# Kernel tuning notes

Measured on AMD Instinct MI355X. Metric: run time of the kernel, lower is better.

## Reference

```python
import jax, jax.numpy as jnp
import numpy as np


def setup_inputs() -> dict:
    key = jax.random.key(0)
    kq, kk, kv, km = jax.random.split(key, 4)
    B, H, S, D = 2, 16, 2048, 64
    q = jax.random.normal(kq, (B, H, S, D), dtype=jnp.float32)
    k = jax.random.normal(kk, (B, H, S, D), dtype=jnp.float32)
    v = jax.random.normal(kv, (B, H, S, D), dtype=jnp.float32)
    mask = jax.random.randint(km, (B, 1, S, S), 0, 2, dtype=jnp.int32)
    return {"q": q, "k": k, "v": v, "mask": mask}


def reference(q, k, v, mask):
    # Scaled dot-product attention: softmax(Q K^T / sqrt(D)) V
    D = q.shape[-1]
    scale = jnp.asarray(1.0 / np.sqrt(D), q.dtype)
    score = jnp.einsum("bhqd,bhkd->bhqk", q, k) * scale  # [B,H,S,S]
    score = jnp.where(mask == 0, jnp.asarray(-10000.0, score.dtype), score)
    attn = jax.nn.softmax(score, axis=-1)
    out = jnp.einsum("bhqk,bhkd->bhqd", attn, v)  # [B,H,S,D]
    return (out, attn)
```

## Files before the change

kernel.cpp:

```cpp
#include <hip/hip_runtime.h>
#include <stdint.h>

typedef __attribute__((ext_vector_type(8))) short short8;
typedef __attribute__((ext_vector_type(4))) float f32x4;

#define B_ 2
#define H_ 16
#define S_ 2048
#define D_ 64

__device__ __forceinline__ short f2b(float f) {
  unsigned u = __builtin_bit_cast(unsigned, f);
  u += 0x7fffu + ((u >> 16) & 1u);
  return (short)(u >> 16);
}

__global__ __launch_bounds__(256, 4)
void attn_kernel(const float* __restrict__ Q, const float* __restrict__ K,
                 const float* __restrict__ V, const int* __restrict__ M,
                 float* __restrict__ O, float* __restrict__ A)
{
  const int qt   = blockIdx.x;
  const int bh   = blockIdx.y;
  const int b    = bh >> 4;
  const int tid  = threadIdx.x;
  const int wave = tid >> 6;
  const int lane = tid & 63;
  const int l15  = lane & 15;
  const int quad = lane >> 4;

  const float* Qp = Q + (size_t)bh * S_ * D_;
  const float* Kp = K + (size_t)bh * S_ * D_;
  const float* Vp = V + (size_t)bh * S_ * D_;
  const int*   Mp = M + (size_t)b * S_ * S_;
  float* Op = O + (size_t)bh * S_ * D_;
  float* Ap = A + (size_t)bh * S_ * S_;

  const int q0 = qt * 64 + wave * 16;

  __shared__ __attribute__((aligned(16))) short Ks[32][72];
  __shared__ __attribute__((aligned(16))) short Vt[64][40];
  __shared__ __attribute__((aligned(16))) short Ps[4][16][40];

  short8 aq[2];
  {
    const float* qr = Qp + (size_t)(q0 + l15) * D_ + quad * 8;
#pragma unroll
    for (int h = 0; h < 2; ++h) {
      const float4 x0 = *(const float4*)(qr + h * 32);
      const float4 x1 = *(const float4*)(qr + h * 32 + 4);
      aq[h][0] = f2b(x0.x * 0.125f); aq[h][1] = f2b(x0.y * 0.125f);
      aq[h][2] = f2b(x0.z * 0.125f); aq[h][3] = f2b(x0.w * 0.125f);
      aq[h][4] = f2b(x1.x * 0.125f); aq[h][5] = f2b(x1.y * 0.125f);
      aq[h][6] = f2b(x1.z * 0.125f); aq[h][7] = f2b(x1.w * 0.125f);
    }
  }

  const int srow = tid >> 3;
  const int sdc  = (tid & 7) * 8;

  float lsum[4] = {0.f, 0.f, 0.f, 0.f};
  for (int kt = 0; kt < S_; kt += 32) {
    __syncthreads();
    {
      const float* kr = Kp + (size_t)(kt + srow) * D_ + sdc;
      const float4 x0 = *(const float4*)(kr);
      const float4 x1 = *(const float4*)(kr + 4);
      short8 t;
      t[0]=f2b(x0.x); t[1]=f2b(x0.y); t[2]=f2b(x0.z); t[3]=f2b(x0.w);
      t[4]=f2b(x1.x); t[5]=f2b(x1.y); t[6]=f2b(x1.z); t[7]=f2b(x1.w);
      *(short8*)&Ks[srow][sdc] = t;
    }
    __syncthreads();

    f32x4 acc[2] = {{0.f,0.f,0.f,0.f},{0.f,0.f,0.f,0.f}};
#pragma unroll
    for (int nt = 0; nt < 2; ++nt)
#pragma unroll
      for (int h = 0; h < 2; ++h) {
        const short8 bk = *(const short8*)&Ks[nt*16 + l15][h*32 + quad*8];
        acc[nt] = __builtin_amdgcn_mfma_f32_16x16x32_bf16(aq[h], bk, acc[nt], 0, 0, 0);
      }
#pragma unroll
    for (int nt = 0; nt < 2; ++nt)
#pragma unroll
      for (int r = 0; r < 4; ++r) {
        const int row = q0 + quad*4 + r;
        const int col = kt + nt*16 + l15;
        const int m = Mp[(size_t)row * S_ + col];
        lsum[r] += m ? __expf(acc[nt][r]) : 0.f;
      }
  }
#pragma unroll
  for (int r = 0; r < 4; ++r) {
    float s = lsum[r];
    s += __shfl_xor(s, 1);
    s += __shfl_xor(s, 2);
    s += __shfl_xor(s, 4);
    s += __shfl_xor(s, 8);
    lsum[r] = (s > 0.f) ? (1.f / s) : 0.f;
  }

  f32x4 oacc[4] = {{0.f,0.f,0.f,0.f},{0.f,0.f,0.f,0.f},
                   {0.f,0.f,0.f,0.f},{0.f,0.f,0.f,0.f}};

  for (int kt = 0; kt < S_; kt += 32) {
    __syncthreads();
    {
      const float* kr = Kp + (size_t)(kt + srow) * D_ + sdc;
      const float4 x0 = *(const float4*)(kr);
      const float4 x1 = *(const float4*)(kr + 4);
      short8 t;
      t[0]=f2b(x0.x); t[1]=f2b(x0.y); t[2]=f2b(x0.z); t[3]=f2b(x0.w);
      t[4]=f2b(x1.x); t[5]=f2b(x1.y); t[6]=f2b(x1.z); t[7]=f2b(x1.w);
      *(short8*)&Ks[srow][sdc] = t;

      const float* vr = Vp + (size_t)(kt + srow) * D_ + sdc;
      const float4 y0 = *(const float4*)(vr);
      const float4 y1 = *(const float4*)(vr + 4);
      Vt[sdc + 0][srow] = f2b(y0.x);
      Vt[sdc + 1][srow] = f2b(y0.y);
      Vt[sdc + 2][srow] = f2b(y0.z);
      Vt[sdc + 3][srow] = f2b(y0.w);
      Vt[sdc + 4][srow] = f2b(y1.x);
      Vt[sdc + 5][srow] = f2b(y1.y);
      Vt[sdc + 6][srow] = f2b(y1.z);
      Vt[sdc + 7][srow] = f2b(y1.w);
    }
    __syncthreads();

    f32x4 acc[2] = {{0.f,0.f,0.f,0.f},{0.f,0.f,0.f,0.f}};
#pragma unroll
    for (int nt = 0; nt < 2; ++nt)
#pragma unroll
      for (int h = 0; h < 2; ++h) {
        const short8 bk = *(const short8*)&Ks[nt*16 + l15][h*32 + quad*8];
        acc[nt] = __builtin_amdgcn_mfma_f32_16x16x32_bf16(aq[h], bk, acc[nt], 0, 0, 0);
      }

#pragma unroll
    for (int nt = 0; nt < 2; ++nt)
#pragma unroll
      for (int r = 0; r < 4; ++r) {
        const int row = q0 + quad*4 + r;
        const int col = kt + nt*16 + l15;
        const int m = Mp[(size_t)row * S_ + col];
        const float p = m ? __expf(acc[nt][r]) * lsum[r] : 0.f;
        Ap[(size_t)row * S_ + col] = p;
        Ps[wave][quad*4 + r][nt*16 + l15] = f2b(p);
      }
    __asm__ volatile("s_waitcnt lgkmcnt(0)" ::: "memory");

    const short8 ap = *(const short8*)&Ps[wave][l15][quad*8];
#pragma unroll
    for (int nt = 0; nt < 4; ++nt) {
      const short8 bv = *(const short8*)&Vt[nt*16 + l15][quad*8];
      oacc[nt] = __builtin_amdgcn_mfma_f32_16x16x32_bf16(ap, bv, oacc[nt], 0, 0, 0);
    }
  }

#pragma unroll
  for (int nt = 0; nt < 4; ++nt)
#pragma unroll
    for (int r = 0; r < 4; ++r)
      Op[(size_t)(q0 + quad*4 + r) * D_ + nt*16 + l15] = oacc[nt][r];
}

extern "C" void kernel_launch(void* const* d_in, const int* in_sizes, int n_in,
                              void* d_out, int out_size, void* d_ws, size_t ws_size,
                              hipStream_t stream) {
  const float* q = (const float*)d_in[0];
  const float* k = (const float*)d_in[1];
  const float* v = (const float*)d_in[2];
  const int*   m = (const int*)d_in[3];
  float* out  = (float*)d_out;
  float* attn = out + (size_t)B_ * H_ * S_ * D_;

  dim3 grid(S_ / 64, B_ * H_);
  attn_kernel<<<grid, 256, 0, stream>>>(q, k, v, m, out, attn);
}
```

Measured before the change: 836.9 us.

## Rewrite attention kernel with 64-key tiles, register prefetch, and vectorized mask/attn I/O

Doubles the key tile to 64, prefetches the next K/V tile into registers while computing the current one, and stages scores through shared memory so each lane handles 4 contiguous columns. Mask loads become int4 and attention-probability stores become nontemporal float4, replacing scattered scalar accesses. Block indices are remapped so neighbouring blocks share a batch-head, bf16 conversion uses a cheaper packed round-half-up, and normalisation folds a log-sum into the exponent. It costs more shared memory and registers and adds extra LDS round trips and barriers.

```diff
diff --git a/kernel.cpp b/kernel.cpp
--- a/kernel.cpp
+++ b/kernel.cpp
@@ -8,11 +8,15 @@
 #define H_ 16
 #define S_ 2048
 #define D_ 64
-
-__device__ __forceinline__ short f2b(float f) {
-  unsigned u = __builtin_bit_cast(unsigned, f);
-  u += 0x7fffu + ((u >> 16) & 1u);
-  return (short)(u >> 16);
+#define KB_ 64
+#define NT_ (S_ / KB_)
+
+union PKU { unsigned u[4]; short8 s; };
+
+__device__ __forceinline__ unsigned pk2(float x, float y) {
+  const unsigned a = __builtin_bit_cast(unsigned, x) + 0x8000u;
+  const unsigned b = __builtin_bit_cast(unsigned, y) + 0x8000u;
+  return (a >> 16) | (b & 0xffff0000u);
 }
 
 __global__ __launch_bounds__(256, 4)
@@ -20,9 +24,11 @@
                  const float* __restrict__ V, const int* __restrict__ M,
                  float* __restrict__ O, float* __restrict__ A)
 {
-  const int qt   = blockIdx.x;
-  const int bh   = blockIdx.y;
-  const int b    = bh >> 4;
+  const int bid = blockIdx.x + (blockIdx.y << 5);
+  const int qt  = (bid >> 3) & 31;
+  const int bh  = (bid & 7) | ((bid >> 8) << 3);
+  const int b   = bh >> 4;
+
   const int tid  = threadIdx.x;
   const int wave = tid >> 6;
   const int lane = tid & 63;
@@ -38,9 +44,10 @@
 
   const int q0 = qt * 64 + wave * 16;
 
-  __shared__ __attribute__((aligned(16))) short Ks[32][72];
-  __shared__ __attribute__((aligned(16))) short Vt[64][40];
-  __shared__ __attribute__((aligned(16))) short Ps[4][16][40];
+  __shared__ __attribute__((aligned(16))) short Ks[64][72];
+  __shared__ __attribute__((aligned(16))) short Vt[64][72];
+  __shared__ __attribute__((aligned(16))) float Ps[4][16][68];
+  short* Pb = (short*)&Ps[wave][0][0];
 
   short8 aq[2];
   {
@@ -49,114 +56,166 @@
     for (int h = 0; h < 2; ++h) {
       const float4 x0 = *(const float4*)(qr + h * 32);
       const float4 x1 = *(const float4*)(qr + h * 32 + 4);
-      aq[h][0] = f2b(x0.x * 0.125f); aq[h][1] = f2b(x0.y * 0.125f);
-      aq[h][2] = f2b(x0.z * 0.125f); aq[h][3] = f2b(x0.w * 0.125f);
-      aq[h][4] = f2b(x1.x * 0.125f); aq[h][5] = f2b(x1.y * 0.125f);
-      aq[h][6] = f2b(x1.z * 0.125f); aq[h][7] = f2b(x1.w * 0.125f);
+      PKU u;
+      u.u[0] = pk2(x0.x * 0.125f, x0.y * 0.125f);
+      u.u[1] = pk2(x0.z * 0.125f, x0.w * 0.125f);
+      u.u[2] = pk2(x1.x * 0.125f, x1.y * 0.125f);
+      u.u[3] = pk2(x1.z * 0.125f, x1.w * 0.125f);
+      aq[h] = u.s;
     }
   }
 
-  const int srow = tid >> 3;
-  const int sdc  = (tid & 7) * 8;
-
-  float lsum[4] = {0.f, 0.f, 0.f, 0.f};
-  for (int kt = 0; kt < S_; kt += 32) {
+  const int ksr  = tid >> 2;
+  const int ksc  = (tid & 3) * 4;
+  const int vd   = tid & 7;
+  const int vk   = (tid >> 3) * 2;
+  const int lrow = lane >> 4;
+  const int lcol = (lane & 15) * 4;
+
+  float kbuf[16];
+  float vbuf[16];
+
+  auto loadK = [&](int kt) {
+#pragma unroll
+    for (int j = 0; j < 4; ++j) {
+      const float4 x = *(const float4*)(Kp + (size_t)(kt + ksr) * D_ + ksc + 16 * j);
+      kbuf[4*j+0] = x.x; kbuf[4*j+1] = x.y; kbuf[4*j+2] = x.z; kbuf[4*j+3] = x.w;
+    }
+  };
+  auto writeK = [&]() {
+#pragma unroll
+    for (int j = 0; j < 4; ++j)
+      *(uint2*)&Ks[ksr][ksc + 16*j] =
+        make_uint2(pk2(kbuf[4*j+0], kbuf[4*j+1]), pk2(kbuf[4*j+2], kbuf[4*j+3]));
+  };
+  auto loadV = [&](int kt) {
+    const float* vr = Vp + (size_t)(kt + vk) * D_ + vd;
+#pragma unroll
+    for (int j = 0; j < 8; ++j) {
+      vbuf[j]   = vr[8*j];
+      vbuf[8+j] = vr[D_ + 8*j];
+    }
+  };
+  auto writeV = [&]() {
+#pragma unroll
+    for (int j = 0; j < 8; ++j)
+      *(unsigned*)&Vt[vd + 8*j][vk] = pk2(vbuf[j], vbuf[8+j]);
+  };
+
+  float lr[4];
+
+  {
+    float rowsum[4] = {0.f, 0.f, 0.f, 0.f};
+    loadK(0);
+    writeK();
     __syncthreads();
-    {
-      const float* kr = Kp + (size_t)(kt + srow) * D_ + sdc;
-      const float4 x0 = *(const float4*)(kr);
-      const float4 x1 = *(const float4*)(kr + 4);
-      short8 t;
-      t[0]=f2b(x0.x); t[1]=f2b(x0.y); t[2]=f2b(x0.z); t[3]=f2b(x0.w);
-      t[4]=f2b(x1.x); t[5]=f2b(x1.y); t[6]=f2b(x1.z); t[7]=f2b(x1.w);
-      *(short8*)&Ks[srow][sdc] = t;
-    }
-    __syncthreads();
-
-    f32x4 acc[2] = {{0.f,0.f,0.f,0.f},{0.f,0.f,0.f,0.f}};
-#pragma unroll
-    for (int nt = 0; nt < 2; ++nt)
+    for (int t = 0; t < NT_; ++t) {
+      const int kt = t * KB_;
+      if (t + 1 < NT_) loadK(kt + KB_);
+      int4 mr[4];
+#pragma unroll
+      for (int i = 0; i < 4; ++i)
+        mr[i] = *(const int4*)(Mp + (size_t)(q0 + lrow + 4*i) * S_ + kt + lcol);
+
+      f32x4 acc[4] = {{0,0,0,0},{0,0,0,0},{0,0,0,0},{0,0,0,0}};
+#pragma unroll
+      for (int nt = 0; nt < 4; ++nt)
+#pragma unroll
+        for (int h = 0; h < 2; ++h) {
+          const short8 bk = *(const short8*)&Ks[nt*16 + l15][h*32 + quad*8];
+          acc[nt] = __builtin_amdgcn_mfma_f32_16x16x32_bf16(aq[h], bk, acc[nt], 0, 0, 0);
+        }
+#pragma unroll
+      for (int nt = 0; nt < 4; ++nt)
+#pragma unroll
+        for (int r = 0; r < 4; ++r)
+          Ps[wave][quad*4 + r][nt*16 + l15] = acc[nt][r];
+      __asm__ volatile("s_waitcnt lgkmcnt(0)" ::: "memory");
+#pragma unroll
+      for (int i = 0; i < 4; ++i) {
+        const f32x4 s = *(const f32x4*)&Ps[wave][lrow + 4*i][lcol];
+        const float e0 = mr[i].x ? __expf(s[0]) : 0.f;
+        const float e1 = mr[i].y ? __expf(s[1]) : 0.f;
+        const float e2 = mr[i].z ? __expf(s[2]) : 0.f;
+        const float e3 = mr[i].w ? __expf(s[3]) : 0.f;
+        rowsum[i] += (e0 + e1) + (e2 + e3);
+      }
+      __syncthreads();
+      if (t + 1 < NT_) writeK();
+      __syncthreads();
+    }
+#pragma unroll
+    for (int i = 0; i < 4; ++i) {
+      float s = rowsum[i];
+      s += __shfl_xor(s, 1);
+      s += __shfl_xor(s, 2);
+      s += __shfl_xor(s, 4);
+      s += __shfl_xor(s, 8);
+      lr[i] = (s > 0.f) ? -__logf(s) : 0.f;
+    }
+  }
+
+  f32x4 oacc[4] = {{0,0,0,0},{0,0,0,0},{0,0,0,0},{0,0,0,0}};
+  loadK(0);
+  loadV(0);
+  writeK();
+  writeV();
+  __syncthreads();
+  for (int t = 0; t < NT_; ++t) {
+    const int kt = t * KB_;
+    if (t + 1 < NT_) { loadK(kt + KB_); loadV(kt + KB_); }
+    int4 mr[4];
+#pragma unroll
+    for (int i = 0; i < 4; ++i)
+      mr[i] = *(const int4*)(Mp + (size_t)(q0 + lrow + 4*i) * S_ + kt + lcol);
+
+    f32x4 acc[4] = {{0,0,0,0},{0,0,0,0},{0,0,0,0},{0,0,0,0}};
+#pragma unroll
+    for (int nt = 0; nt < 4; ++nt)
 #pragma unroll
       for (int h = 0; h < 2; ++h) {
         const short8 bk = *(const short8*)&Ks[nt*16 + l15][h*32 + quad*8];
         acc[nt] = __builtin_amdgcn_mfma_f32_16x16x32_bf16(aq[h], bk, acc[nt], 0, 0, 0);
       }
 #pragma unroll
-    for (int nt = 0; nt < 2; ++nt)
-#pragma unroll
-      for (int r = 0; r < 4; ++r) {
-        const int row = q0 + quad*4 + r;
-        const int col = kt + nt*16 + l15;
-        const int m = Mp[(size_t)row * S_ + col];
-        lsum[r] += m ? __expf(acc[nt][r]) : 0.f;
-      }
-  }
-#pragma unroll
-  for (int r = 0; r < 4; ++r) {
-    float s = lsum[r];
-    s += __shfl_xor(s, 1);
-    s += __shfl_xor(s, 2);
-    s += __shfl_xor(s, 4);
-    s += __shfl_xor(s, 8);
-    lsum[r] = (s > 0.f) ? (1.f / s) : 0.f;
-  }
-
-  f32x4 oacc[4] = {{0.f,0.f,0.f,0.f},{0.f,0.f,0.f,0.f},
-                   {0.f,0.f,0.f,0.f},{0.f,0.f,0.f,0.f}};
-
-  for (int kt = 0; kt < S_; kt += 32) {
+    for (int nt = 0; nt < 4; ++nt)
+#pragma unroll
+      for (int r = 0; r < 4; ++r)
+        Ps[wave][quad*4 + r][nt*16 + l15] = acc[nt][r];
+    __asm__ volatile("s_waitcnt lgkmcnt(0)" ::: "memory");
+
+    f32x4 sr[4];
+#pragma unroll
+    for (int i = 0; i < 4; ++i)
+      sr[i] = *(const f32x4*)&Ps[wave][lrow + 4*i][lcol];
+    __asm__ volatile("s_waitcnt lgkmcnt(0)" ::: "memory");
+
+#pragma unroll
+    for (int i = 0; i < 4; ++i) {
+      const float lv = lr[i];
+      f32x4 p;
+      p[0] = __expf(mr[i].x ? sr[i][0] + lv : -1e5f);
+      p[1] = __expf(mr[i].y ? sr[i][1] + lv : -1e5f);
+      p[2] = __expf(mr[i].z ? sr[i][2] + lv : -1e5f);
+      p[3] = __expf(mr[i].w ? sr[i][3] + lv : -1e5f);
+      __builtin_nontemporal_store(p, (f32x4*)(Ap + (size_t)(q0 + lrow + 4*i) * S_ + kt + lcol));
+      *(uint2*)&Pb[(lrow + 4*i) * 72 + lcol] =
+        make_uint2(pk2(p[0], p[1]), pk2(p[2], p[3]));
+    }
+    __asm__ volatile("s_waitcnt lgkmcnt(0)" ::: "memory");
+
+    const short8 pa0 = *(const short8*)&Pb[l15 * 72 + quad * 8];
+    const short8 pa1 = *(const short8*)&Pb[l15 * 72 + 32 + quad * 8];
+#pragma unroll
+    for (int nt = 0; nt < 4; ++nt) {
+      const short8 bv0 = *(const short8*)&Vt[nt*16 + l15][quad*8];
+      const short8 bv1 = *(const short8*)&Vt[nt*16 + l15][32 + quad*8];
+      oacc[nt] = __builtin_amdgcn_mfma_f32_16x16x32_bf16(pa0, bv0, oacc[nt], 0, 0, 0);
+      oacc[nt] = __builtin_amdgcn_mfma_f32_16x16x32_bf16(pa1, bv1, oacc[nt], 0, 0, 0);
+    }
     __syncthreads();
-    {
-      const float* kr = Kp + (size_t)(kt + srow) * D_ + sdc;
-      const float4 x0 = *(const float4*)(kr);
-      const float4 x1 = *(const float4*)(kr + 4);
-      short8 t;
-      t[0]=f2b(x0.x); t[1]=f2b(x0.y); t[2]=f2b(x0.z); t[3]=f2b(x0.w);
-      t[4]=f2b(x1.x); t[5]=f2b(x1.y); t[6]=f2b(x1.z); t[7]=f2b(x1.w);
-      *(short8*)&Ks[srow][sdc] = t;
-
-      const float* vr = Vp + (size_t)(kt + srow) * D_ + sdc;
-      const float4 y0 = *(const float4*)(vr);
-      const float4 y1 = *(const float4*)(vr + 4);
-      Vt[sdc + 0][srow] = f2b(y0.x);
-      Vt[sdc + 1][srow] = f2b(y0.y);
-      Vt[sdc + 2][srow] = f2b(y0.z);
-      Vt[sdc + 3][srow] = f2b(y0.w);
-      Vt[sdc + 4][srow] = f2b(y1.x);
-      Vt[sdc + 5][srow] = f2b(y1.y);
-      Vt[sdc + 6][srow] = f2b(y1.z);
-      Vt[sdc + 7][srow] = f2b(y1.w);
-    }
+    if (t + 1 < NT_) { writeK(); writeV(); }
     __syncthreads();
-
-    f32x4 acc[2] = {{0.f,0.f,0.f,0.f},{0.f,0.f,0.f,0.f}};
-#pragma unroll
-    for (int nt = 0; nt < 2; ++nt)
-#pragma unroll
-      for (int h = 0; h < 2; ++h) {
-        const short8 bk = *(const short8*)&Ks[nt*16 + l15][h*32 + quad*8];
-        acc[nt] = __builtin_amdgcn_mfma_f32_16x16x32_bf16(aq[h], bk, acc[nt], 0, 0, 0);
-      }
-
-#pragma unroll
-    for (int nt = 0; nt < 2; ++nt)
-#pragma unroll
-      for (int r = 0; r < 4; ++r) {
-        const int row = q0 + quad*4 + r;
-        const int col = kt + nt*16 + l15;
-        const int m = Mp[(size_t)row * S_ + col];
-        const float p = m ? __expf(acc[nt][r]) * lsum[r] : 0.f;
-        Ap[(size_t)row * S_ + col] = p;
-        Ps[wave][quad*4 + r][nt*16 + l15] = f2b(p);
-      }
-    __asm__ volatile("s_waitcnt lgkmcnt(0)" ::: "memory");
-
-    const short8 ap = *(const short8*)&Ps[wave][l15][quad*8];
-#pragma unroll
-    for (int nt = 0; nt < 4; ++nt) {
-      const short8 bv = *(const short8*)&Vt[nt*16 + l15][quad*8];
-      oacc[nt] = __builtin_amdgcn_mfma_f32_16x16x32_bf16(ap, bv, oacc[nt], 0, 0, 0);
-    }
   }
 
 #pragma unroll
```

After: 731.1 us. 12.6% less time.
